# Optimization experiments

Hardware: AMD Instinct MI355X
Metric: run time of the kernel (lower is better)

The kernel has to match this reference:

```python
import jax, jax.numpy as jnp
import numpy as np

N = 100000       # nodes
E = 1600000      # edges
NFEAT = 128
NHID = 128
NCLASS = 64
NHEAD = 4
NLAYER = 3
LRELU_ALPHA = 0.2


def setup_inputs() -> dict:
    key = jax.random.key(0)
    ks = jax.random.split(key, 7)
    x = jax.random.normal(ks[0], (N, NFEAT), jnp.float32)
    edge_index = jax.random.randint(ks[1], (2, E), 0, N, jnp.int32)
    # xavier-uniform-ish init scales (gain for relu baked into scale roughly)
    Win = jax.random.normal(ks[2], (NFEAT, NHID), jnp.float32) * (2.0 / (NFEAT + NHID)) ** 0.5
    b_in = jnp.zeros((NHID,), jnp.float32)
    # per hidden layer, per head: a split into (src, dst) halves of the (1, 2*in) vector
    a_hid = jax.random.normal(ks[3], (NLAYER - 1, NHEAD, 2, NHID), jnp.float32) * 0.1
    W_hid = jax.random.normal(ks[4], (NLAYER - 1, NHEAD, NHID, NHID // NHEAD), jnp.float32) * (2.0 / (NHID + NHID // NHEAD)) ** 0.5
    a_out = jax.random.normal(ks[5], (2, NHID), jnp.float32) * 0.1
    W_out = jax.random.normal(ks[6], (NHID, NCLASS), jnp.float32) * (2.0 / (NHID + NCLASS)) ** 0.5
    return dict(x=x, edge_index=edge_index, Win=Win, b_in=b_in,
                a_hid=a_hid, W_hid=W_hid, a_out=a_out, W_out=W_out)


def _segment_softmax(logits, seg, n):
    # numerically stable softmax over groups defined by seg (axis 0)
    m = jax.ops.segment_max(logits, seg, num_segments=n)
    e = jnp.exp(logits - m[seg])
    s = jax.ops.segment_sum(e, seg, num_segments=n)
    return e / s[seg]


def _gat_conv(h, row, col, a, W):
    # h: [N, D]; a: [H, 2, D]; W: [H, D, Dh]
    n = h.shape[0]
    H = a.shape[0]
    s_src = h @ a[:, 0, :].T  # [N, H]
    s_dst = h @ a[:, 1, :].T  # [N, H]
    logits = jax.nn.leaky_relu(s_src[row] + s_dst[col], LRELU_ALPHA)  # [E, H]
    alpha = _segment_softmax(logits, row, n)  # softmax grouped by row (edge_index[0])
    h_col = h[col]  # [E, D] gathered once, reused per head
    outs = []
    for hd in range(H):  # small fixed head loop keeps peak memory at [E, D]
        agg = jax.ops.segment_sum(alpha[:, hd, None] * h_col, row, num_segments=n)  # [N, D]
        outs.append(agg @ W[hd])  # weight applied AFTER aggregation, as in source
    return jnp.concatenate(outs, axis=1)


def reference(x, edge_index, Win, b_in, a_hid, W_hid, a_out, W_out):
    row, col = edge_index[0], edge_index[1]
    h = jax.nn.elu(x @ Win + b_in)  # in_linear + ELU (dropout is identity in eval/p=0)
    for l in range(a_hid.shape[0]):
        h = jax.nn.elu(_gat_conv(h, row, col, a_hid[l], W_hid[l]))
    # final conv: single head to nclass, no activation
    return _gat_conv(h, row, col, a_out[None], W_out[None])
```

## Files before the change

### kernel.cpp

```cpp
#include <hip/hip_runtime.h>
#include <hip/hip_bf16.h>
#include <cstdint>
#include <cstddef>

#define LRELU_ALPHA 0.2f
#define LOG2E 1.44269504088896f

typedef __attribute__((ext_vector_type(8))) short short8;
typedef __attribute__((ext_vector_type(4))) float f32x4;
typedef _Float16 h2v __attribute__((ext_vector_type(2)));

__device__ __forceinline__ unsigned short f2bf(float f) {
    unsigned int u = __float_as_uint(f);
    unsigned int r = (u + 0x7fffu + ((u >> 16) & 1u)) >> 16;
    return (unsigned short)r;
}
__device__ __forceinline__ float bf2f(unsigned int lo16) {
    return __uint_as_float(lo16 << 16);
}
__device__ __forceinline__ unsigned int pk2(float a, float b) {
    return (unsigned int)f2bf(a) | ((unsigned int)f2bf(b) << 16);
}
__device__ __forceinline__ float fexp2(float x) {
#if __has_builtin(__builtin_amdgcn_exp2f)
    return __builtin_amdgcn_exp2f(x);
#else
    return __expf(x * 0.69314718056f);
#endif
}
__device__ __forceinline__ h2v pkrtz(float a, float b) {
#if __has_builtin(__builtin_amdgcn_cvt_pkrtz)
    auto r = __builtin_amdgcn_cvt_pkrtz(a, b);
    union { decltype(r) i; h2v o; } u;
    u.i = r;
    return u.o;
#else
    h2v r; r.x = (_Float16)a; r.y = (_Float16)b; return r;
#endif
}
__device__ __forceinline__ unsigned int pack_lo(unsigned int a, unsigned int b) {
#if __has_builtin(__builtin_amdgcn_perm)
    return __builtin_amdgcn_perm(a, b, 0x01000504u);
#else
    return (a & 0xffffu) | (b << 16);
#endif
}
__device__ __forceinline__ unsigned int pack_hi(unsigned int a, unsigned int b) {
#if __has_builtin(__builtin_amdgcn_perm)
    return __builtin_amdgcn_perm(a, b, 0x03020706u);
#else
    return (a >> 16) | (b & 0xffff0000u);
#endif
}
union U32H2 { unsigned int u; h2v h; };
__device__ __forceinline__ float dot2f(unsigned int a, h2v w, float acc) {
    U32H2 c; c.u = a;
#if __has_builtin(__builtin_amdgcn_fdot2)
    return __builtin_amdgcn_fdot2(c.h, w, acc, false);
#else
    return acc + (float)c.h.x * (float)w.x + (float)c.h.y * (float)w.y;
#endif
}


__global__ void hist_k(const int* __restrict__ ei, int* __restrict__ counts,
                       int* __restrict__ rank, int E_) {
    int e = blockIdx.x * 256 + threadIdx.x;
    if (e < E_) {
        int r = ei[e];
        rank[e] = atomicAdd(&counts[r], 1);
    }
}

__global__ void fill_pad_k(int* __restrict__ scol, float* __restrict__ sdA,
                           float* __restrict__ sdB, float* __restrict__ sdC,
                           unsigned int* __restrict__ hW, int N_, int total) {
    int i = blockIdx.x * 256 + threadIdx.x;
    if (i < total) scol[i] = N_;
    if (blockIdx.x == 0) {
        int t = threadIdx.x;
        if (t < 4) { sdA[N_ * 4 + t] = -1e30f; sdB[N_ * 4 + t] = -1e30f; }
        if (t == 4) sdC[N_] = -1e30f;
        if (t >= 32 && t < 64)  hW[(size_t)N_ * 32 + (t - 32)] = 0u;
        if (t >= 64 && t < 128) hW[(size_t)N_ * 64 + (t - 64)] = 0u;
    }
}

__global__ void scan_block_k(const int* __restrict__ counts, int* __restrict__ tmp,
                             int* __restrict__ bsum, int n) {
    __shared__ int s[256];
    int i = blockIdx.x * 256 + threadIdx.x;
    int v = (i < n) ? ((counts[i] + 7) & ~7) : 0;
    s[threadIdx.x] = v;
    __syncthreads();
    for (int d = 1; d < 256; d <<= 1) {
        int t_ = (threadIdx.x >= d) ? s[threadIdx.x - d] : 0;
        __syncthreads();
        s[threadIdx.x] += t_;
        __syncthreads();
    }
    if (i < n) tmp[i] = s[threadIdx.x];
    if (threadIdx.x == 255) bsum[blockIdx.x] = s[255];
}

__global__ void scan_sums_k(int* bsum, int nb) {
    __shared__ int s[512];
    int v = ((int)threadIdx.x < nb) ? bsum[threadIdx.x] : 0;
    s[threadIdx.x] = v;
    __syncthreads();
    for (int d = 1; d < 512; d <<= 1) {
        int t_ = ((int)threadIdx.x >= d) ? s[threadIdx.x - d] : 0;
        __syncthreads();
        s[threadIdx.x] += t_;
        __syncthreads();
    }
    if ((int)threadIdx.x < nb) bsum[threadIdx.x] = s[threadIdx.x] - v;
}

__global__ void finalize_k(const int* __restrict__ tmp, const int* __restrict__ bsum,
                           int* __restrict__ off, int n) {
    int i = blockIdx.x * 256 + threadIdx.x;
    if (i < n) off[i + 1] = tmp[i] + bsum[blockIdx.x];
    if (i == 0) off[0] = 0;
}

__global__ void scatter_k(const int* __restrict__ ei, const int* __restrict__ rank,
                          const int* __restrict__ off, int* __restrict__ scol, int E_) {
    int e = blockIdx.x * 256 + threadIdx.x;
    if (e < E_) {
        int r = ei[e];
        int pos = off[r] + rank[e];
        scol[pos] = ei[E_ + e];
    }
}


__global__ void repack_all(const float* __restrict__ Win, const float* __restrict__ Whid,
                           const float* __restrict__ Wout,
                           unsigned short* __restrict__ W0, unsigned short* __restrict__ W1,
                           unsigned short* __restrict__ W2, unsigned short* __restrict__ W3) {
    int i = blockIdx.x * 256 + threadIdx.x;
    if (i < 16384) {
        int n = i >> 7, k = i & 127;
        W0[i] = f2bf(Win[k * 128 + n]);
    } else if (i < 49152) {
        int j = i - 16384;
        int l = j >> 14;
        int jj = j & 16383;
        int n = jj >> 7, k = jj & 127;
        int hd = n >> 5, c = n & 31;
        float v = Whid[(size_t)l * 16384 + (hd * 128 + k) * 32 + c];
        (l ? W2 : W1)[jj] = f2bf(v);
    } else if (i < 57344) {
        int j = i - 49152;
        int n = j >> 7, k = j & 127;
        W3[j] = f2bf(Wout[k * 64 + n]);
    }
}


template <int KJ, bool ELU_ACT, bool BIAS, int OUTM, bool ABF16>
__global__ __launch_bounds__(256) void gemm_mfma(const void* __restrict__ Xv,
                                                 const unsigned short* __restrict__ WT,
                                                 const float* __restrict__ bias,
                                                 void* __restrict__ Yv, int nRows) {
    constexpr int NT = KJ / 16;
    constexpr int WS = 136;
    __shared__ unsigned short sWT[KJ * WS];
    int t = threadIdx.x;
    for (int i = t; i < KJ * 16; i += 256) {
        int n = i >> 4, k8 = i & 15;
        uint4 v = *(const uint4*)&WT[n * 128 + k8 * 8];
        *(uint4*)&sWT[n * WS + k8 * 8] = v;
    }
    __syncthreads();

    int lane = t & 63;
    int wv = t >> 6;
    int m0 = blockIdx.x * 128 + wv * 32;
    int l16 = lane & 15;
    int q4 = lane >> 4;

    short8 afr[4][2];
    #pragma unroll
    for (int rt = 0; rt < 2; rt++) {
        int row = m0 + rt * 16 + l16;
        bool vr = row < nRows;
        if (ABF16) {
            const unsigned int* xp = (const unsigned int*)Xv + (size_t)row * 64 + q4 * 4;
            #pragma unroll
            for (int kk = 0; kk < 4; kk++) {
                uint4 u = make_uint4(0u, 0u, 0u, 0u);
                if (vr) u = *(const uint4*)(xp + kk * 16);
                afr[kk][rt] = *(short8*)&u;
            }
        } else {
            const float* xp = (const float*)Xv + (size_t)row * 128 + q4 * 8;
            #pragma unroll
            for (int kk = 0; kk < 4; kk++) {
                float4 a0 = make_float4(0.f, 0.f, 0.f, 0.f), a1 = a0;
                if (vr) {
                    a0 = *(const float4*)(xp + kk * 32);
                    a1 = *(const float4*)(xp + kk * 32 + 4);
                }
                unsigned int u[4];
                u[0] = pk2(a0.x, a0.y); u[1] = pk2(a0.z, a0.w);
                u[2] = pk2(a1.x, a1.y); u[3] = pk2(a1.z, a1.w);
                afr[kk][rt] = *(short8*)u;
            }
        }
    }

    f32x4 acc[2][NT] = {};
    #pragma unroll
    for (int kk = 0; kk < 4; kk++) {
        #pragma unroll
        for (int ct = 0; ct < NT; ct++) {
            int n = ct * 16 + l16;
            short8 bf = *(const short8*)&sWT[n * WS + kk * 32 + q4 * 8];
            #pragma unroll
            for (int rt = 0; rt < 2; rt++)
                acc[rt][ct] = __builtin_amdgcn_mfma_f32_16x16x32_bf16(afr[kk][rt], bf, acc[rt][ct], 0, 0, 0);
        }
    }

    #pragma unroll
    for (int rt = 0; rt < 2; rt++) {
        #pragma unroll
        for (int q = 0; q < 4; q++) {
            int row = m0 + rt * 16 + q4 * 4 + q;
            if (row >= nRows) continue;
            #pragma unroll
            for (int ct = 0; ct < NT; ct++) {
                int colc = ct * 16 + l16;
                float v = acc[rt][ct][q];
                if (BIAS) v += bias[colc];
                if (ELU_ACT) v = v > 0.f ? v : (__expf(v) - 1.f);
                if (OUTM == 1) {
                    ((unsigned short*)Yv)[(size_t)row * KJ + colc] = f2bf(v);
                } else if (OUTM == 2) {
                    union { _Float16 hf; unsigned short us; } cv;
                    cv.hf = (_Float16)v;
                    ((unsigned short*)Yv)[(size_t)row * KJ + colc] = cv.us;
                } else {
                    ((float*)Yv)[(size_t)row * KJ + colc] = v;
                }
            }
        }
    }
}


template <int H>
__global__ __launch_bounds__(256) void attn_scores16(const unsigned int* __restrict__ h2,
                                                     const float* __restrict__ a,
                                                     float* __restrict__ s_src,
                                                     float* __restrict__ s_dst, int n) {
    __shared__ float sa[H * 2 * 128];
    for (int i = threadIdx.x; i < H * 2 * 128; i += 256) sa[i] = a[i] * LOG2E;
    __syncthreads();
    int lane = threadIdx.x & 63, wv = threadIdx.x >> 6;
    int sub = lane & 15, g = lane >> 4;
    int node = (blockIdx.x * 4 + wv) * 4 + g;
    bool valid = node < n;
    int nd = valid ? node : 0;
    uint4 hv = *(const uint4*)&h2[(size_t)nd * 64 + sub * 4];
    float f[8];
    f[0] = bf2f(hv.x & 0xffffu); f[1] = bf2f(hv.x >> 16);
    f[2] = bf2f(hv.y & 0xffffu); f[3] = bf2f(hv.y >> 16);
    f[4] = bf2f(hv.z & 0xffffu); f[5] = bf2f(hv.z >> 16);
    f[6] = bf2f(hv.w & 0xffffu); f[7] = bf2f(hv.w >> 16);
    #pragma unroll
    for (int c = 0; c < 2 * H; c++) {
        const float* ap = &sa[c * 128 + sub * 8];
        float p = 0.f;
        #pragma unroll
        for (int q = 0; q < 8; q++) p += f[q] * ap[q];
        #pragma unroll
        for (int s = 1; s < 16; s <<= 1) p += __shfl_xor(p, s);
        if (sub == 0 && valid) {
            float* dst = (c & 1) ? s_dst : s_src;
            dst[node * H + (c >> 1)] = p;
        }
    }
}


template <int DHT, int H, bool ELU_ACT, int HN, bool BF16O>
__global__ __launch_bounds__(256) void edge_agg_v(const unsigned int* __restrict__ hW2,
                                                  const float* __restrict__ ssrc,
                                                  const float* __restrict__ sdst,
                                                  const int* __restrict__ off,
                                                  const int* __restrict__ scol,
                                                  void* __restrict__ outv,
                                                  const float* __restrict__ a_next,
                                                  float* __restrict__ ssrc_n,
                                                  float* __restrict__ sdst_n, int nRows) {
    constexpr int FPL = DHT / 16;
    constexpr int UPL = FPL / 2;
    constexpr int NC = (HN > 0) ? 2 * HN : 1;
    __shared__ float sAN[NC * 128];
    if (HN > 0) {
        for (int i = threadIdx.x; i < NC * 128; i += 256) sAN[i] = a_next[i] * LOG2E;
        __syncthreads();
    }
    int lane = threadIdx.x & 63;
    int sub = lane & 15;
    int g = lane >> 4;
    int wv = threadIdx.x >> 6;
    int r = __builtin_amdgcn_readfirstlane(blockIdx.x * 4 + wv);
    if (r >= nRows) return;
    int begin = off[r], end = off[r + 1];

    int head = (H == 4) ? (sub >> 2) : 0;
    float ssl = ssrc[r * H + head];

    float acc[FPL] = {};
    float den = 0.f;

    for (int i = begin; i < end; i += 8) {
        int2 cc = *(const int2*)&scol[i + 2 * g];
        int cA = cc.x, cB = cc.y;
        float sdA = sdst[cA * H + head];
        float sdB = sdst[cB * H + head];
        unsigned int hA[UPL], hB[UPL];
        int oA = cA * (DHT / 2) + sub * UPL;
        int oB = cB * (DHT / 2) + sub * UPL;
        if (UPL == 4) {
            *(uint4*)hA = *(const uint4*)&hW2[oA];
            *(uint4*)hB = *(const uint4*)&hW2[oB];
        } else {
            *(uint2*)hA = *(const uint2*)&hW2[oA];
            *(uint2*)hB = *(const uint2*)&hW2[oB];
        }
        float lgA = ssl + sdA;
        float wA = fexp2(fmaxf(lgA, LRELU_ALPHA * lgA));
        float lgB = ssl + sdB;
        float wB = fexp2(fmaxf(lgB, LRELU_ALPHA * lgB));
        den += wA + wB;
        h2v w2 = pkrtz(wA, wB);
        #pragma unroll
        for (int q = 0; q < UPL; q++) {
            acc[2 * q]     = dot2f(pack_lo(hA[q], hB[q]), w2, acc[2 * q]);
            acc[2 * q + 1] = dot2f(pack_hi(hA[q], hB[q]), w2, acc[2 * q + 1]);
        }
    }

    #pragma unroll
    for (int s = 16; s < 64; s <<= 1) {
        den += __shfl_xor(den, s);
        #pragma unroll
        for (int p = 0; p < FPL; p++) acc[p] += __shfl_xor(acc[p], s);
    }
    float inv = den > 0.f ? 1.f / den : 0.f;

    float v[FPL];
    #pragma unroll
    for (int p = 0; p < FPL; p++) {
        float tv = acc[p] * inv;
        if (ELU_ACT) tv = tv > 0.f ? tv : (__expf(tv) - 1.f);
        v[p] = tv;
    }

    if (DHT == 128) {
        if (BF16O)
            ((unsigned int*)outv)[(size_t)r * 64 + sub * 4 + g] = pk2(v[2 * g], v[2 * g + 1]);
        else
            *(float2*)&((float*)outv)[(size_t)r * 128 + sub * 8 + 2 * g] =
                make_float2(v[2 * g], v[2 * g + 1]);
    } else {
        ((float*)outv)[(size_t)r * DHT + sub * FPL + g] = v[g];
    }

    if (HN > 0) {
        constexpr int CPG = (HN == 4) ? 2 : 1;
        #pragma unroll
        for (int cc = 0; cc < CPG; cc++) {
            int c = (HN == 4) ? (g * 2 + cc) : (g & 1);
            const float* ap = &sAN[c * 128 + sub * FPL];
            float partial = 0.f;
            #pragma unroll
            for (int p = 0; p < FPL; p++) partial += v[p] * ap[p];
            #pragma unroll
            for (int s = 1; s < 16; s <<= 1) partial += __shfl_xor(partial, s);
            if (sub == 0 && (HN == 4 || g < 2)) {
                int hd = c >> 1;
                float* dst = (c & 1) ? sdst_n : ssrc_n;
                dst[r * HN + hd] = partial;
            }
        }
    }
}


extern "C" void kernel_launch(void* const* d_in, const int* in_sizes, int n_in,
                              void* d_out, int out_size, void* d_ws, size_t ws_size,
                              hipStream_t stream) {
    const float* x    = (const float*)d_in[0];
    const int*   ei   = (const int*)d_in[1];
    const float* Win  = (const float*)d_in[2];
    const float* bin  = (const float*)d_in[3];
    const float* ahid = (const float*)d_in[4];
    const float* Whid = (const float*)d_in[5];
    const float* aout = (const float*)d_in[6];
    const float* Wout = (const float*)d_in[7];
    float* out = (float*)d_out;

    const int N_ = in_sizes[0] / 128;
    const int E_ = in_sizes[1] / 2;

    char* p = (char*)d_ws;
    auto alloc = [&](size_t bytes) {
        char* q = p;
        p += (bytes + 511) & ~(size_t)511;
        return q;
    };
    int* counts = (int*)alloc((size_t)N_ * 4);
    int* tmp    = (int*)alloc((size_t)N_ * 4);
    int* rank   = (int*)alloc((size_t)E_ * 4);
    int* off    = (int*)alloc((size_t)(N_ + 1) * 4);
    int* bsum   = (int*)alloc(4096);
    int* scol   = (int*)alloc((size_t)(E_ + 8 * N_ + 64) * 4);
    float* ssrcA = (float*)alloc((size_t)(N_ + 1) * 4 * 4);
    float* sdstA = (float*)alloc((size_t)(N_ + 1) * 4 * 4);
    float* ssrcB = (float*)alloc((size_t)(N_ + 1) * 4 * 4);
    float* sdstB = (float*)alloc((size_t)(N_ + 1) * 4 * 4);
    float* ssrcC = (float*)alloc((size_t)(N_ + 1) * 4);
    float* sdstC = (float*)alloc((size_t)(N_ + 1) * 4);
    unsigned int* hb  = (unsigned int*)alloc((size_t)N_ * 64 * 4);
    unsigned int* hWb = (unsigned int*)alloc((size_t)(N_ + 1) * 64 * 4);
    unsigned short* WT0 = (unsigned short*)alloc(128 * 128 * 2);
    unsigned short* WT1 = (unsigned short*)alloc(128 * 128 * 2);
    unsigned short* WT2 = (unsigned short*)alloc(128 * 128 * 2);
    unsigned short* WT3 = (unsigned short*)alloc(64 * 128 * 2);

    int NB = (N_ + 255) / 256;
    int EB = (E_ + 255) / 256;
    int RT = (N_ + 127) / 128;
    int NW = (N_ + 3) / 4;
    int PADTOT = E_ + 8 * N_;

    (void)hipMemsetAsync(counts, 0, (size_t)N_ * 4, stream);
    hist_k<<<EB, 256, 0, stream>>>(ei, counts, rank, E_);
    fill_pad_k<<<(PADTOT + 255) / 256, 256, 0, stream>>>(scol, sdstA, sdstB, sdstC, hWb, N_, PADTOT);
    scan_block_k<<<NB, 256, 0, stream>>>(counts, tmp, bsum, N_);
    scan_sums_k<<<1, 512, 0, stream>>>(bsum, NB);
    finalize_k<<<NB, 256, 0, stream>>>(tmp, bsum, off, N_);
    scatter_k<<<EB, 256, 0, stream>>>(ei, rank, off, scol, E_);

    repack_all<<<224, 256, 0, stream>>>(Win, Whid, Wout, WT0, WT1, WT2, WT3);

    gemm_mfma<128, true, true, 1, false><<<RT, 256, 0, stream>>>(x, WT0, bin, hb, N_);

    attn_scores16<4><<<(N_ + 15) / 16, 256, 0, stream>>>(hb, ahid, ssrcA, sdstA, N_);

    gemm_mfma<128, false, false, 2, true><<<RT, 256, 0, stream>>>(hb, WT1, nullptr, hWb, N_);
    edge_agg_v<128, 4, true, 4, true><<<NW, 256, 0, stream>>>(
        hWb, ssrcA, sdstA, off, scol, hb, ahid + 4 * 2 * 128, ssrcB, sdstB, N_);

    gemm_mfma<128, false, false, 2, true><<<RT, 256, 0, stream>>>(hb, WT2, nullptr, hWb, N_);
    edge_agg_v<128, 4, true, 1, true><<<NW, 256, 0, stream>>>(
        hWb, ssrcB, sdstB, off, scol, hb, aout, ssrcC, sdstC, N_);

    gemm_mfma<64, false, false, 2, true><<<RT, 256, 0, stream>>>(hb, WT3, nullptr, hWb, N_);
    edge_agg_v<64, 1, false, 0, false><<<NW, 256, 0, stream>>>(
        hWb, ssrcC, sdstC, off, scol, out, nullptr, nullptr, nullptr, N_);
}
```

Measured before the change: 480.8 us.

## Unfuse next-layer attention scores from edge aggregation; merge histogram with pad fill

The next-layer attention score computation is moved out of the edge aggregation kernel and into separate attn_scores16 launches that read the bf16 hidden output. This removes the shared-memory staging, block barrier and extra shuffles from the aggregation kernel, but adds two launches and an extra pass over the hidden features. Separately, the histogram kernel and the padding-fill kernel are merged into one launch. Scores are now computed from the bf16-rounded hidden values rather than the fp32 values, which slightly changes numerics.

```diff
diff --git a/kernel.cpp b/kernel.cpp
--- a/kernel.cpp
+++ b/kernel.cpp
@@ -63,20 +63,17 @@
 }
 
 
-__global__ void hist_k(const int* __restrict__ ei, int* __restrict__ counts,
-                       int* __restrict__ rank, int E_) {
-    int e = blockIdx.x * 256 + threadIdx.x;
-    if (e < E_) {
-        int r = ei[e];
-        rank[e] = atomicAdd(&counts[r], 1);
-    }
-}
-
-__global__ void fill_pad_k(int* __restrict__ scol, float* __restrict__ sdA,
-                           float* __restrict__ sdB, float* __restrict__ sdC,
-                           unsigned int* __restrict__ hW, int N_, int total) {
+__global__ void fill_hist_k(const int* __restrict__ ei, int* __restrict__ counts,
+                            int* __restrict__ rank, int* __restrict__ scol,
+                            float* __restrict__ sdA, float* __restrict__ sdB,
+                            float* __restrict__ sdC, unsigned int* __restrict__ hW,
+                            int N_, int E_, int total) {
     int i = blockIdx.x * 256 + threadIdx.x;
     if (i < total) scol[i] = N_;
+    if (i < E_) {
+        int r = ei[i];
+        rank[i] = atomicAdd(&counts[r], 1);
+    }
     if (blockIdx.x == 0) {
         int t = threadIdx.x;
         if (t < 4) { sdA[N_ * 4 + t] = -1e30f; sdB[N_ * 4 + t] = -1e30f; }
@@ -286,24 +283,15 @@
 }
 
 
-template <int DHT, int H, bool ELU_ACT, int HN, bool BF16O>
+template <int DHT, int H, bool ELU_ACT, bool BF16O>
 __global__ __launch_bounds__(256) void edge_agg_v(const unsigned int* __restrict__ hW2,
                                                   const float* __restrict__ ssrc,
                                                   const float* __restrict__ sdst,
                                                   const int* __restrict__ off,
                                                   const int* __restrict__ scol,
-                                                  void* __restrict__ outv,
-                                                  const float* __restrict__ a_next,
-                                                  float* __restrict__ ssrc_n,
-                                                  float* __restrict__ sdst_n, int nRows) {
+                                                  void* __restrict__ outv, int nRows) {
     constexpr int FPL = DHT / 16;
     constexpr int UPL = FPL / 2;
-    constexpr int NC = (HN > 0) ? 2 * HN : 1;
-    __shared__ float sAN[NC * 128];
-    if (HN > 0) {
-        for (int i = threadIdx.x; i < NC * 128; i += 256) sAN[i] = a_next[i] * LOG2E;
-        __syncthreads();
-    }
     int lane = threadIdx.x & 63;
     int sub = lane & 15;
     int g = lane >> 4;
@@ -370,25 +358,6 @@
                 make_float2(v[2 * g], v[2 * g + 1]);
     } else {
         ((float*)outv)[(size_t)r * DHT + sub * FPL + g] = v[g];
-    }
-
-    if (HN > 0) {
-        constexpr int CPG = (HN == 4) ? 2 : 1;
-        #pragma unroll
-        for (int cc = 0; cc < CPG; cc++) {
-            int c = (HN == 4) ? (g * 2 + cc) : (g & 1);
-            const float* ap = &sAN[c * 128 + sub * FPL];
-            float partial = 0.f;
-            #pragma unroll
-            for (int p = 0; p < FPL; p++) partial += v[p] * ap[p];
-            #pragma unroll
-            for (int s = 1; s < 16; s <<= 1) partial += __shfl_xor(partial, s);
-            if (sub == 0 && (HN == 4 || g < 2)) {
-                int hd = c >> 1;
-                float* dst = (c & 1) ? sdst_n : ssrc_n;
-                dst[r * HN + hd] = partial;
-            }
-        }
     }
 }
 
@@ -438,11 +407,12 @@
     int EB = (E_ + 255) / 256;
     int RT = (N_ + 127) / 128;
     int NW = (N_ + 3) / 4;
+    int NS = (N_ + 15) / 16;
     int PADTOT = E_ + 8 * N_;
 
     (void)hipMemsetAsync(counts, 0, (size_t)N_ * 4, stream);
-    hist_k<<<EB, 256, 0, stream>>>(ei, counts, rank, E_);
-    fill_pad_k<<<(PADTOT + 255) / 256, 256, 0, stream>>>(scol, sdstA, sdstB, sdstC, hWb, N_, PADTOT);
+    fill_hist_k<<<(PADTOT + 255) / 256, 256, 0, stream>>>(
+        ei, counts, rank, scol, sdstA, sdstB, sdstC, hWb, N_, E_, PADTOT);
     scan_block_k<<<NB, 256, 0, stream>>>(counts, tmp, bsum, N_);
     scan_sums_k<<<1, 512, 0, stream>>>(bsum, NB);
     finalize_k<<<NB, 256, 0, stream>>>(tmp, bsum, off, N_);
@@ -452,17 +422,19 @@
 
     gemm_mfma<128, true, true, 1, false><<<RT, 256, 0, stream>>>(x, WT0, bin, hb, N_);
 
-    attn_scores16<4><<<(N_ + 15) / 16, 256, 0, stream>>>(hb, ahid, ssrcA, sdstA, N_);
+    attn_scores16<4><<<NS, 256, 0, stream>>>(hb, ahid, ssrcA, sdstA, N_);
 
     gemm_mfma<128, false, false, 2, true><<<RT, 256, 0, stream>>>(hb, WT1, nullptr, hWb, N_);
-    edge_agg_v<128, 4, true, 4, true><<<NW, 256, 0, stream>>>(
-        hWb, ssrcA, sdstA, off, scol, hb, ahid + 4 * 2 * 128, ssrcB, sdstB, N_);
+    edge_agg_v<128, 4, true, true><<<NW, 256, 0, stream>>>(
+        hWb, ssrcA, sdstA, off, scol, hb, N_);
+    attn_scores16<4><<<NS, 256, 0, stream>>>(hb, ahid + 4 * 2 * 128, ssrcB, sdstB, N_);
 
     gemm_mfma<128, false, false, 2, true><<<RT, 256, 0, stream>>>(hb, WT2, nullptr, hWb, N_);
-    edge_agg_v<128, 4, true, 1, true><<<NW, 256, 0, stream>>>(
-        hWb, ssrcB, sdstB, off, scol, hb, aout, ssrcC, sdstC, N_);
+    edge_agg_v<128, 4, true, true><<<NW, 256, 0, stream>>>(
+        hWb, ssrcB, sdstB, off, scol, hb, N_);
+    attn_scores16<1><<<NS, 256, 0, stream>>>(hb, aout, ssrcC, sdstC, N_);
 
     gemm_mfma<64, false, false, 2, true><<<RT, 256, 0, stream>>>(hb, WT3, nullptr, hWb, N_);
-    edge_agg_v<64, 1, false, 0, false><<<NW, 256, 0, stream>>>(
-        hWb, ssrcC, sdstC, off, scol, out, nullptr, nullptr, nullptr, N_);
-}
+    edge_agg_v<64, 1, false, false><<<NW, 256, 0, stream>>>(
+        hWb, ssrcC, sdstC, off, scol, out, N_);
+}
```

Result: no change. 483.5 us (+0.5%).
